# Kernel tuning notes

Hardware: AMD Instinct MI355X
Metric: run time of the kernel (lower is better)

## Reference

```python
import jax, jax.numpy as jnp
import numpy as np

NUM_CLASSES = 91
VARIANCES = jnp.asarray([0.1, 0.1, 0.2, 0.2], dtype=jnp.float32)
FG_THRES = 0.5
BG_HI = 0.5
BG_LO = 0.1
ROIS_PER_IMAGE = 256
POS_RATIO = 0.25
N_ROI = 200000
N_GT = 200


def _make_boxes(key, n):
    # random valid normalized y1,x1,y2,x2 boxes
    kc, ks = jax.random.split(key)
    c = jax.random.uniform(kc, (n, 2))                      # centers (cy,cx)
    hw = jax.random.uniform(ks, (n, 2), minval=0.02, maxval=0.3)
    lo = jnp.clip(c - hw / 2, 0.0, 1.0)
    hi = jnp.clip(c + hw / 2, 0.0, 1.0)
    return jnp.concatenate([lo, hi], axis=1).astype(jnp.float32)


def setup_inputs() -> dict:
    key = jax.random.key(0)
    kg, kr, ki, kn, kl = jax.random.split(key, 5)
    gt = _make_boxes(kg, N_GT)
    # first chunk of rois are jittered GT boxes so positives exist
    n_jit = 5000
    idx = jax.random.randint(ki, (n_jit,), 0, N_GT)
    noise = jax.random.normal(kn, (n_jit, 4)) * 0.02
    jit = jnp.clip(gt[idx] + noise, 0.0, 1.0)
    jit = jnp.concatenate([jnp.minimum(jit[:, :2], jit[:, 2:]),
                           jnp.maximum(jit[:, :2], jit[:, 2:])], axis=1)
    rnd = _make_boxes(kr, N_ROI - n_jit)
    rois = jnp.concatenate([jit, rnd], axis=0)
    gt_labels = jax.random.randint(kl, (1, N_GT), 1, NUM_CLASSES).astype(jnp.int32)
    return {
        "img_shape": jnp.asarray([1024, 1024], dtype=jnp.int32),
        "roi_bboxes": rois[None],          # [1, N_ROI, 4]
        "gt_boxes": gt[None],              # [1, N_GT, 4]
        "gt_labels": gt_labels,            # [1, N_GT]
    }


def _pairwise_iou(a, b):
    # a: [N,4], b: [M,4], boxes are (y1,x1,y2,x2) -> [N,M]
    iy1 = jnp.maximum(a[:, None, 0], b[None, :, 0])
    ix1 = jnp.maximum(a[:, None, 1], b[None, :, 1])
    iy2 = jnp.minimum(a[:, None, 2], b[None, :, 2])
    ix2 = jnp.minimum(a[:, None, 3], b[None, :, 3])
    inter = jnp.clip(iy2 - iy1, 0.0) * jnp.clip(ix2 - ix1, 0.0)
    area_a = (a[:, 2] - a[:, 0]) * (a[:, 3] - a[:, 1])
    area_b = (b[:, 2] - b[:, 0]) * (b[:, 3] - b[:, 1])
    union = area_a[:, None] + area_b[None, :] - inter
    return inter / (union + 1e-7)


def _get_deltas(bboxes, gt):
    bh = bboxes[:, 2] - bboxes[:, 0]
    bw = bboxes[:, 3] - bboxes[:, 1]
    bcy = bboxes[:, 0] + 0.5 * bh
    bcx = bboxes[:, 1] + 0.5 * bw
    gh = gt[:, 2] - gt[:, 0]
    gw = gt[:, 3] - gt[:, 1]
    gcy = gt[:, 0] + 0.5 * gh
    gcx = gt[:, 1] + 0.5 * gw
    bh_s = jnp.where(bh == 0, 1.0, bh)
    bw_s = jnp.where(bw == 0, 1.0, bw)
    gh_s = jnp.where(gh <= 0, 1.0, gh)
    gw_s = jnp.where(gw <= 0, 1.0, gw)
    dy = jnp.where(gh == 0, 0.0, (gcy - bcy) / bh_s)
    dx = jnp.where(gw == 0, 0.0, (gcx - bcx) / bw_s)
    dh = jnp.where(gh == 0, 0.0, jnp.log(gh_s / bh_s))
    dw = jnp.where(gw == 0, 0.0, jnp.log(gw_s / bw_s))
    return jnp.stack([dy, dx, dh, dw], axis=-1)


def reference(img_shape, roi_bboxes, gt_boxes, gt_labels):
    rois = roi_bboxes[0]           # [N,4]
    gts = gt_boxes[0]              # [M,4]
    labels = gt_labels[0]          # [M]

    iou = _pairwise_iou(rois, gts)             # [N,M] -- dominant memory traffic
    best_gt = jnp.argmax(iou, axis=1)          # [N]
    merged = jnp.max(iou, axis=1)              # [N]

    pos = merged > FG_THRES
    neg = (merged < BG_HI) & (merged > BG_LO)

    max_pos = jnp.int32(round(ROIS_PER_IMAGE * POS_RATIO))
    total_pos = jnp.minimum(max_pos, pos.sum())
    total_neg = jnp.minimum(ROIS_PER_IMAGE - total_pos, neg.sum())

    # deterministic take-first-k selection (stand-in for randomly_select_xyz_mask)
    pos_sel = pos & (jnp.cumsum(pos.astype(jnp.int32)) <= total_pos)
    neg_sel = neg & (jnp.cumsum(neg.astype(jnp.int32)) <= total_neg)

    # stable sort key: positives first, then negatives, then unselected
    key_arr = jnp.where(pos_sel, 0, jnp.where(neg_sel, 1, 2)).astype(jnp.int32)
    order = jnp.argsort(key_arr, stable=True)[:ROIS_PER_IMAGE]   # [R]
    valid = key_arr[order] < 2                                   # [R]
    is_pos = pos_sel[order]                                      # [R]

    rois_s = rois[order]                                         # [R,4]
    gt_s = jnp.where(is_pos[:, None], gts[best_gt[order]], 0.0)  # expanded_gt_boxes
    lab_s = jnp.where(is_pos & valid, labels[best_gt[order]], 0) # pos->cls, neg/pad->0

    deltas = (_get_deltas(rois_s, gt_s) / VARIANCES) * valid[:, None]
    onehot = jax.nn.one_hot(lab_s, NUM_CLASSES, dtype=jnp.float32) * valid[:, None]
    return deltas[None], onehot[None]   # [1,R,4], [1,R,NUM_CLASSES]
```

## Files before the change

kernel.cpp:

```cpp
#include <hip/hip_runtime.h>
#include <cstdint>

static constexpr int RPI    = 256;
static constexpr int MAXPOS = 64;
static constexpr int MAXNEG = RPI - MAXPOS;
static constexpr int MAX_GT = 256;
static constexpr int MAXG   = 4096;
static constexpr int NBLK_A = 64;
static constexpr int NBF    = 64;

static constexpr size_t WS_CNT    = 0;
static constexpr size_t WS_GRPPK  = 64;
static constexpr size_t WS_BESTGT = WS_GRPPK + (size_t)MAXG * 4;
static constexpr size_t WS_KEY    = WS_BESTGT + (size_t)262144 * 2;

struct IouSmem {
    float4 sgt[MAX_GT];
    float  sarea[MAX_GT];
    float  sabe[MAX_GT];
    float  sbi[4][64];
    float  sc1[4][64];
    short  sbj[4][64];
};

__device__ __forceinline__ void stage_gt(
    IouSmem& S, const float* __restrict__ gts, int M)
{
#pragma clang fp contract(off)
    const int tid = threadIdx.x;
    for (int j = tid; j < M; j += 256) {
        float4 g = ((const float4*)gts)[j];
        S.sgt[j] = g;
        float a = (g.z - g.x) * (g.w - g.y);
        S.sarea[j] = a;
        S.sabe[j]  = a + 1e-7f;
    }
    __syncthreads();
}

__device__ __forceinline__ void iou_tile(
    IouSmem& S, const float* __restrict__ rois,
    int N, int M, int blk,
    uint8_t* __restrict__ key, int16_t* __restrict__ bestgt,
    int* __restrict__ grpPk)
{
#pragma clang fp contract(off)
    const int tid = threadIdx.x;
    const int w = tid >> 6, l = tid & 63;
    const int base = blk * 64;
    const int r = base + l;
    const float4 zb = make_float4(0.f, 0.f, 0.f, 0.f);
    float4 b = (r < N) ? ((const float4*)rois)[r] : zb;
    float aA = (b.z - b.x) * (b.w - b.y);

    const int seglen = (M + 3) >> 2;
    const int j0 = w * seglen, j1 = min(M, j0 + seglen);

    float bi = -1.f, c1 = 0.f;
    int   bj = j0;

    float4 g0 = S.sgt[j0],     g1 = S.sgt[j0 + 1];
    float  a0 = S.sabe[j0],    a1 = S.sabe[j0 + 1];
#pragma unroll 2
    for (int j = j0; j < j1; ++j) {
        float4 gn = S.sgt[j + 2];
        float  an = S.sabe[j + 2];
        float ih = fmaxf(fminf(b.z, g0.z) - fmaxf(b.x, g0.x), 0.f);
        float iw = fmaxf(fminf(b.w, g0.w) - fmaxf(b.y, g0.y), 0.f);
        float inter = ih * iw;
        float Sx = aA + a0;
        bool  s = (inter * c1) > (bi * Sx);
        bi = s ? inter : bi;  c1 = s ? Sx : c1;  bj = s ? j : bj;
        g0 = g1; a0 = a1; g1 = gn; a1 = an;
    }
    S.sbi[w][l] = bi;  S.sc1[w][l] = c1;  S.sbj[w][l] = (short)bj;
    __syncthreads();

    if (tid < 64) {
        float BI = S.sbi[0][tid], C1 = S.sc1[0][tid];
        int   BJ = (int)S.sbj[0][tid];
#pragma unroll
        for (int s2 = 1; s2 < 4; ++s2) {
            float ci = S.sbi[s2][tid], cc = S.sc1[s2][tid];
            bool sel = (ci * C1) > (BI * cc);
            BI = sel ? ci : BI;  C1 = sel ? cc : C1;
            BJ = sel ? (int)S.sbj[s2][tid] : BJ;
        }
        int rr = base + tid;
        int kk = 2;
        if (rr < N) {
            float4 gg = S.sgt[BJ];
            float  ab = S.sarea[BJ];
            float ih = fmaxf(fminf(b.z, gg.z) - fmaxf(b.x, gg.x), 0.f);
            float iw = fmaxf(fminf(b.w, gg.w) - fmaxf(b.y, gg.y), 0.f);
            float inter = ih * iw;
            float u1 = ((aA + ab) - inter) + 1e-7f;
            float q  = inter / u1;
            kk = (q > 0.5f) ? 0 : ((q < 0.5f && q > 0.1f) ? 1 : 2);
            key[rr]    = (uint8_t)kk;
            bestgt[rr] = (int16_t)BJ;
        }
        unsigned long long mp = __ballot(kk == 0);
        unsigned long long mn = __ballot(kk == 1);
        if (tid == 0)
            grpPk[blk] = (__popcll(mp) << 16) | __popcll(mn);
    }
    __syncthreads();
}

__device__ __forceinline__ void emit_row(
    int row, int roi, int tp, int l,
    const float* __restrict__ rois, const float* __restrict__ gts,
    const int* __restrict__ labels, const int16_t* __restrict__ bestgt,
    float* __restrict__ outD, float* __restrict__ outH)
{
#pragma clang fp contract(off)
    bool valid = roi >= 0;
    bool ispos = valid && (row < tp);
    float d0 = 0.f, d1 = 0.f, d2 = 0.f, d3 = 0.f;
    int lab = valid ? 0 : -1;
    if (ispos) {
        int gi    = (int)bestgt[roi];
        float4 b  = ((const float4*)rois)[roi];
        float4 gb = ((const float4*)gts)[gi];
        lab = labels[gi];
        float bh  = b.z - b.x,  bw  = b.w - b.y;
        float bcy = b.x + 0.5f * bh, bcx = b.y + 0.5f * bw;
        float gh  = gb.z - gb.x, gw  = gb.w - gb.y;
        float gcy = gb.x + 0.5f * gh, gcx = gb.y + 0.5f * gw;
        float bhs = (bh == 0.f) ? 1.f : bh;
        float bws = (bw == 0.f) ? 1.f : bw;
        float ghs = (gh <= 0.f) ? 1.f : gh;
        float gws = (gw <= 0.f) ? 1.f : gw;
        float dy = (gh == 0.f) ? 0.f : (gcy - bcy) / bhs;
        float dx = (gw == 0.f) ? 0.f : (gcx - bcx) / bws;
        float dh = (gh == 0.f) ? 0.f : logf(ghs / bhs);
        float dw = (gw == 0.f) ? 0.f : logf(gws / bws);
        d0 = dy / 0.1f; d1 = dx / 0.1f; d2 = dh / 0.2f; d3 = dw / 0.2f;
    }
    if (l == 0) ((float4*)outD)[row] = make_float4(d0, d1, d2, d3);
    outH[row * 91 + l] = (l == lab) ? 1.0f : 0.0f;
    if (l < 27) outH[row * 91 + 64 + l] = ((64 + l) == lab) ? 1.0f : 0.0f;
}

__global__ __launch_bounds__(256) void iouA_kernel(
    const float* __restrict__ rois, const float* __restrict__ gts,
    int N, int M,
    uint8_t* __restrict__ key, int16_t* __restrict__ bestgt,
    int* __restrict__ grpPk, int* __restrict__ cnt)
{
    __shared__ IouSmem S;
    if (blockIdx.x == 0 && threadIdx.x == 0) cnt[0] = 0;
    stage_gt(S, gts, M);
    iou_tile(S, rois, N, M, (int)blockIdx.x, key, bestgt, grpPk);
}

__global__ __launch_bounds__(256) void gated_kernel(
    const float* __restrict__ rois, const float* __restrict__ gts,
    const int* __restrict__ labels,
    int N, int M,
    uint8_t* __restrict__ key, int16_t* __restrict__ bestgt,
    int* __restrict__ grpPk, int* __restrict__ cnt,
    float* __restrict__ outD, float* __restrict__ outH,
    int kgrp, int nblkC, int nWork, int ngroups)
{
#pragma clang fp contract(off)
    __shared__ IouSmem S;
    __shared__ int slot[RPI];
    __shared__ int redP[4], redN[4];
    __shared__ int wTotP[4], wTotN[4];
    __shared__ int s_fast, s_tp, s_tn;

    const int tid = threadIdx.x, w = tid >> 6, l = tid & 63;

    if (tid < RPI) slot[tid] = -1;
    if (w == 0) {
        int v = (l < kgrp) ? grpPk[l] : 0;
        int p = v >> 16, n = v & 0xFFFF;
#pragma unroll
        for (int o = 1; o < 64; o <<= 1) {
            p += __shfl_xor(p, o);
            n += __shfl_xor(n, o);
        }
        if (l == 0) s_fast = (p >= MAXPOS && n >= MAXNEG) ? 1 : 0;
    }
    __syncthreads();
    const bool fast = s_fast != 0;

    if (fast) {
        const int nk = kgrp * 4;
        int kc[16];
        int p = 0, n = 0;
        if (tid < nk) {
            uint4 kv = ((const uint4*)key)[tid];
            unsigned wd[4] = { kv.x, kv.y, kv.z, kv.w };
            const int i0 = tid * 16;
#pragma unroll
            for (int x = 0; x < 4; ++x)
#pragma unroll
                for (int b = 0; b < 4; ++b) {
                    int i = 4 * x + b;
                    int k = (int)((wd[x] >> (8 * b)) & 0xFF);
                    kc[i] = (i0 + i < N) ? k : 2;
                    p += (kc[i] == 0);
                    n += (kc[i] == 1);
                }
        } else {
#pragma unroll
            for (int i = 0; i < 16; ++i) kc[i] = 2;
        }
        int ip = p, in_ = n;
#pragma unroll
        for (int o = 1; o < 64; o <<= 1) {
            int up = __shfl_up(ip, o), un = __shfl_up(in_, o);
            if (l >= o) { ip += up; in_ += un; }
        }
        if (l == 63) { wTotP[w] = ip; wTotN[w] = in_; }
        __syncthreads();
        int bp = 0, bn = 0;
        for (int x = 0; x < w; ++x) { bp += wTotP[x]; bn += wTotN[x]; }
        int rp = bp + ip - p;
        int rn = bn + in_ - n;
        const int i0 = tid * 16;
#pragma unroll
        for (int i = 0; i < 16; ++i) {
            if (kc[i] == 0)      { if (rp < MAXPOS) slot[rp] = i0 + i; ++rp; }
            else if (kc[i] == 1) { if (rn < MAXNEG) slot[MAXPOS + rn] = i0 + i; ++rn; }
        }
        __syncthreads();
        const int stride = gridDim.x * 4;
        for (int row = (int)blockIdx.x * 4 + w; row < RPI; row += stride)
            emit_row(row, slot[row], MAXPOS, l, rois, gts, labels, bestgt, outD, outH);
        return;
    }

    if ((int)blockIdx.x < nWork) {
        stage_gt(S, gts, M);
        for (int t = (int)blockIdx.x; t < nblkC; t += nWork)
            iou_tile(S, rois, N, M, NBLK_A + t, key, bestgt, grpPk);
        __threadfence();
        __syncthreads();
        if (tid == 0) atomicAdd(cnt, 1);
        return;
    }
    if (tid == 0) { while (atomicAdd(cnt, 0) < nWork) { } }
    __syncthreads();
    __threadfence();

    {
        int sumP = 0, sumN = 0;
        for (int g = tid; g < ngroups; g += 256) {
            int v = grpPk[g];
            sumP += v >> 16;
            sumN += v & 0xFFFF;
        }
#pragma unroll
        for (int o = 32; o > 0; o >>= 1) {
            sumP += __shfl_down(sumP, o);
            sumN += __shfl_down(sumN, o);
        }
        if (l == 0) { redP[w] = sumP; redN[w] = sumN; }
        __syncthreads();
        if (tid == 0) {
            int totP = redP[0] + redP[1] + redP[2] + redP[3];
            int totN = redN[0] + redN[1] + redN[2] + redN[3];
            int tp  = totP < MAXPOS ? totP : MAXPOS;
            int rem = RPI - tp;
            s_tp = tp;
            s_tn = totN < rem ? totN : rem;
        }
    }
    __syncthreads();
    const int tp = s_tp, tn = s_tn;

    if (w == 0) {
        int cp = 0, cn = 0;
        int kc = (l < N) ? (int)key[l] : 2;
        for (int g = 0; g < ngroups && (cp < tp || cn < tn); ++g) {
            int i2 = (g + 1) * 64 + l;
            int kn = (g + 1 < ngroups && i2 < N) ? (int)key[i2] : 2;
            unsigned long long mp = __ballot(kc == 0);
            unsigned long long mn = __ballot(kc == 1);
            unsigned long long lt = (1ull << l) - 1ull;
            int i = g * 64 + l;
            if (kc == 0) {
                int rr = cp + __popcll(mp & lt);
                if (rr < tp) slot[rr] = i;
            } else if (kc == 1) {
                int rr = cn + __popcll(mn & lt);
                if (rr < tn) slot[tp + rr] = i;
            }
            cp += __popcll(mp); cn += __popcll(mn);
            kc = kn;
        }
    }
    __syncthreads();
    for (int row = w; row < RPI; row += 4)
        emit_row(row, slot[row], tp, l, rois, gts, labels, bestgt, outD, outH);
}

extern "C" void kernel_launch(void* const* d_in, const int* in_sizes, int n_in,
                              void* d_out, int out_size, void* d_ws, size_t ws_size,
                              hipStream_t stream) {
    const float* rois   = (const float*)d_in[1];
    const float* gts    = (const float*)d_in[2];
    const int*   labels = (const int*)  d_in[3];
    int N = in_sizes[1] / 4;
    int M = in_sizes[2] / 4;

    char* ws = (char*)d_ws;
    int*     cnt    = (int*)    (ws + WS_CNT);
    int*     grpPk  = (int*)    (ws + WS_GRPPK);
    int16_t* bestgt = (int16_t*)(ws + WS_BESTGT);
    uint8_t* key    = (uint8_t*)(ws + WS_KEY);

    int ngroups = (N + 63) / 64;
    int nblkA   = ngroups < NBLK_A ? ngroups : NBLK_A;
    int kgrp    = nblkA;
    int nblkC   = ngroups - nblkA;
    if (nblkC < 0) nblkC = 0;
    int nWork   = nblkC < NBF ? nblkC : NBF;

    float* outD = (float*)d_out;
    float* outH = outD + RPI * 4;

    iouA_kernel<<<nblkA, 256, 0, stream>>>(rois, gts, N, M, key, bestgt, grpPk, cnt);
    gated_kernel<<<nWork + 1, 256, 0, stream>>>(rois, gts, labels, N, M,
                                                key, bestgt, grpPk, cnt,
                                                outD, outH, kgrp, nblkC, nWork, ngroups);
}
```

Measured before the change: 16.10 us.

## Fuse IoU and selection kernels into one cooperative kernel with grid sync

Replaces the two launches (IoU pass A plus a gated kernel that spins on an atomic counter) with a single cooperative kernel. It uses grid.sync() between the first IoU pass and the fast-path check, and between the fallback IoU tiles and the count reduction. This removes one kernel launch gap and the spin-wait counter. The cost is cooperative-launch overhead and grid-wide barrier latency, and the grid is now capped at nA+1 blocks for the fallback path.

Measured after the change: 44.30 us. 175% more time.

```diff
diff --git a/kernel.cpp b/kernel.cpp
--- a/kernel.cpp
+++ b/kernel.cpp
@@ -1,5 +1,8 @@
 #include <hip/hip_runtime.h>
+#include <hip/hip_cooperative_groups.h>
 #include <cstdint>
+
+namespace cg = cooperative_groups;
 
 static constexpr int RPI    = 256;
 static constexpr int MAXPOS = 64;
@@ -7,10 +10,8 @@
 static constexpr int MAX_GT = 256;
 static constexpr int MAXG   = 4096;
 static constexpr int NBLK_A = 64;
-static constexpr int NBF    = 64;
-
-static constexpr size_t WS_CNT    = 0;
-static constexpr size_t WS_GRPPK  = 64;
+
+static constexpr size_t WS_GRPPK  = 0;
 static constexpr size_t WS_BESTGT = WS_GRPPK + (size_t)MAXG * 4;
 static constexpr size_t WS_KEY    = WS_BESTGT + (size_t)262144 * 2;
 
@@ -143,35 +144,33 @@
     if (l < 27) outH[row * 91 + 64 + l] = ((64 + l) == lab) ? 1.0f : 0.0f;
 }
 
-__global__ __launch_bounds__(256) void iouA_kernel(
-    const float* __restrict__ rois, const float* __restrict__ gts,
-    int N, int M,
-    uint8_t* __restrict__ key, int16_t* __restrict__ bestgt,
-    int* __restrict__ grpPk, int* __restrict__ cnt)
-{
-    __shared__ IouSmem S;
-    if (blockIdx.x == 0 && threadIdx.x == 0) cnt[0] = 0;
-    stage_gt(S, gts, M);
-    iou_tile(S, rois, N, M, (int)blockIdx.x, key, bestgt, grpPk);
-}
-
-__global__ __launch_bounds__(256) void gated_kernel(
+__global__ __launch_bounds__(256) void coop_kernel(
     const float* __restrict__ rois, const float* __restrict__ gts,
     const int* __restrict__ labels,
     int N, int M,
     uint8_t* __restrict__ key, int16_t* __restrict__ bestgt,
-    int* __restrict__ grpPk, int* __restrict__ cnt,
+    int* __restrict__ grpPk,
     float* __restrict__ outD, float* __restrict__ outH,
-    int kgrp, int nblkC, int nWork, int ngroups)
+    int kgrp, int nA, int nblkC, int ngroups)
 {
 #pragma clang fp contract(off)
+    cg::grid_group grid = cg::this_grid();
     __shared__ IouSmem S;
     __shared__ int slot[RPI];
+    __shared__ int wTotP[4], wTotN[4];
     __shared__ int redP[4], redN[4];
-    __shared__ int wTotP[4], wTotN[4];
     __shared__ int s_fast, s_tp, s_tn;
 
     const int tid = threadIdx.x, w = tid >> 6, l = tid & 63;
+    const int bid = (int)blockIdx.x;
+
+    if (bid < nA) {
+        stage_gt(S, gts, M);
+        iou_tile(S, rois, N, M, bid, key, bestgt, grpPk);
+    }
+    __threadfence();
+    grid.sync();
+    __threadfence();
 
     if (tid < RPI) slot[tid] = -1;
     if (w == 0) {
@@ -187,7 +186,9 @@
     __syncthreads();
     const bool fast = s_fast != 0;
 
+    int tp, tn;
     if (fast) {
+        tp = MAXPOS; tn = MAXNEG;
         const int nk = kgrp * 4;
         int kc[16];
         int p = 0, n = 0;
@@ -228,74 +229,66 @@
             else if (kc[i] == 1) { if (rn < MAXNEG) slot[MAXPOS + rn] = i0 + i; ++rn; }
         }
         __syncthreads();
-        const int stride = gridDim.x * 4;
-        for (int row = (int)blockIdx.x * 4 + w; row < RPI; row += stride)
-            emit_row(row, slot[row], MAXPOS, l, rois, gts, labels, bestgt, outD, outH);
-        return;
-    }
-
-    if ((int)blockIdx.x < nWork) {
-        stage_gt(S, gts, M);
-        for (int t = (int)blockIdx.x; t < nblkC; t += nWork)
-            iou_tile(S, rois, N, M, NBLK_A + t, key, bestgt, grpPk);
+    } else {
+        if (bid >= nA) stage_gt(S, gts, M);
+        for (int t = bid; t < nblkC; t += (int)gridDim.x)
+            iou_tile(S, rois, N, M, nA + t, key, bestgt, grpPk);
         __threadfence();
+        grid.sync();
+        __threadfence();
+
+        {
+            int sumP = 0, sumN = 0;
+            for (int g = tid; g < ngroups; g += 256) {
+                int v = grpPk[g];
+                sumP += v >> 16;
+                sumN += v & 0xFFFF;
+            }
+#pragma unroll
+            for (int o = 32; o > 0; o >>= 1) {
+                sumP += __shfl_down(sumP, o);
+                sumN += __shfl_down(sumN, o);
+            }
+            if (l == 0) { redP[w] = sumP; redN[w] = sumN; }
+            __syncthreads();
+            if (tid == 0) {
+                int totP = redP[0] + redP[1] + redP[2] + redP[3];
+                int totN = redN[0] + redN[1] + redN[2] + redN[3];
+                int tpp  = totP < MAXPOS ? totP : MAXPOS;
+                int rem  = RPI - tpp;
+                s_tp = tpp;
+                s_tn = totN < rem ? totN : rem;
+            }
+        }
         __syncthreads();
-        if (tid == 0) atomicAdd(cnt, 1);
-        return;
-    }
-    if (tid == 0) { while (atomicAdd(cnt, 0) < nWork) { } }
-    __syncthreads();
-    __threadfence();
-
-    {
-        int sumP = 0, sumN = 0;
-        for (int g = tid; g < ngroups; g += 256) {
-            int v = grpPk[g];
-            sumP += v >> 16;
-            sumN += v & 0xFFFF;
-        }
-#pragma unroll
-        for (int o = 32; o > 0; o >>= 1) {
-            sumP += __shfl_down(sumP, o);
-            sumN += __shfl_down(sumN, o);
-        }
-        if (l == 0) { redP[w] = sumP; redN[w] = sumN; }
+        tp = s_tp; tn = s_tn;
+
+        if (w == 0) {
+            int cp = 0, cn = 0;
+            int kc = (l < N) ? (int)key[l] : 2;
+            for (int g = 0; g < ngroups && (cp < tp || cn < tn); ++g) {
+                int i2 = (g + 1) * 64 + l;
+                int kn = (g + 1 < ngroups && i2 < N) ? (int)key[i2] : 2;
+                unsigned long long mp = __ballot(kc == 0);
+                unsigned long long mn = __ballot(kc == 1);
+                unsigned long long lt = (1ull << l) - 1ull;
+                int i = g * 64 + l;
+                if (kc == 0) {
+                    int rr = cp + __popcll(mp & lt);
+                    if (rr < tp) slot[rr] = i;
+                } else if (kc == 1) {
+                    int rr = cn + __popcll(mn & lt);
+                    if (rr < tn) slot[tp + rr] = i;
+                }
+                cp += __popcll(mp); cn += __popcll(mn);
+                kc = kn;
+            }
+        }
         __syncthreads();
-        if (tid == 0) {
-            int totP = redP[0] + redP[1] + redP[2] + redP[3];
-            int totN = redN[0] + redN[1] + redN[2] + redN[3];
-            int tp  = totP < MAXPOS ? totP : MAXPOS;
-            int rem = RPI - tp;
-            s_tp = tp;
-            s_tn = totN < rem ? totN : rem;
-        }
-    }
-    __syncthreads();
-    const int tp = s_tp, tn = s_tn;
-
-    if (w == 0) {
-        int cp = 0, cn = 0;
-        int kc = (l < N) ? (int)key[l] : 2;
-        for (int g = 0; g < ngroups && (cp < tp || cn < tn); ++g) {
-            int i2 = (g + 1) * 64 + l;
-            int kn = (g + 1 < ngroups && i2 < N) ? (int)key[i2] : 2;
-            unsigned long long mp = __ballot(kc == 0);
-            unsigned long long mn = __ballot(kc == 1);
-            unsigned long long lt = (1ull << l) - 1ull;
-            int i = g * 64 + l;
-            if (kc == 0) {
-                int rr = cp + __popcll(mp & lt);
-                if (rr < tp) slot[rr] = i;
-            } else if (kc == 1) {
-                int rr = cn + __popcll(mn & lt);
-                if (rr < tn) slot[tp + rr] = i;
-            }
-            cp += __popcll(mp); cn += __popcll(mn);
-            kc = kn;
-        }
-    }
-    __syncthreads();
-    for (int row = w; row < RPI; row += 4)
+    }
+
+    const int stride = (int)gridDim.x * 4;
+    for (int row = bid * 4 + w; row < RPI; row += stride)
         emit_row(row, slot[row], tp, l, rois, gts, labels, bestgt, outD, outH);
 }
 
@@ -309,23 +302,26 @@
     int M = in_sizes[2] / 4;
 
     char* ws = (char*)d_ws;
-    int*     cnt    = (int*)    (ws + WS_CNT);
     int*     grpPk  = (int*)    (ws + WS_GRPPK);
     int16_t* bestgt = (int16_t*)(ws + WS_BESTGT);
     uint8_t* key    = (uint8_t*)(ws + WS_KEY);
 
     int ngroups = (N + 63) / 64;
-    int nblkA   = ngroups < NBLK_A ? ngroups : NBLK_A;
-    int kgrp    = nblkA;
-    int nblkC   = ngroups - nblkA;
+    int nA      = ngroups < NBLK_A ? ngroups : NBLK_A;
+    int kgrp    = nA;
+    int nblkC   = ngroups - nA;
     if (nblkC < 0) nblkC = 0;
-    int nWork   = nblkC < NBF ? nblkC : NBF;
 
     float* outD = (float*)d_out;
     float* outH = outD + RPI * 4;
 
-    iouA_kernel<<<nblkA, 256, 0, stream>>>(rois, gts, N, M, key, bestgt, grpPk, cnt);
-    gated_kernel<<<nWork + 1, 256, 0, stream>>>(rois, gts, labels, N, M,
-                                                key, bestgt, grpPk, cnt,
-                                                outD, outH, kgrp, nblkC, nWork, ngroups);
-}
+    void* args[] = {
+        (void*)&rois, (void*)&gts, (void*)&labels,
+        (void*)&N, (void*)&M,
+        (void*)&key, (void*)&bestgt, (void*)&grpPk,
+        (void*)&outD, (void*)&outH,
+        (void*)&kgrp, (void*)&nA, (void*)&nblkC, (void*)&ngroups
+    };
+    hipLaunchCooperativeKernel((const void*)coop_kernel,
+                               dim3(nA + 1), dim3(256), args, 0, stream);
+}
```
